# Kernel tuning notes

Hardware: AMD Instinct MI355X
Metric: run time of the kernel (lower is better)

Reference implementation:

```python
import jax, jax.numpy as jnp
import numpy as np

EMBED_DIM = 1024
NUM_MEMORY_SLOTS = 256
B, Q = 8, 4096


def setup_inputs() -> dict:
    key = jax.random.key(0)
    ks = jax.random.split(key, 6)
    s = 1.0 / np.sqrt(EMBED_DIM)
    return {
        "x": jax.random.normal(ks[0], (B, Q, EMBED_DIM), dtype=jnp.float32),
        "memory_bank": jax.random.normal(ks[1], (NUM_MEMORY_SLOTS, EMBED_DIM), dtype=jnp.float32),
        "Wq": jax.random.uniform(ks[2], (EMBED_DIM, EMBED_DIM), jnp.float32, -s, s),
        "bq": jax.random.uniform(ks[3], (EMBED_DIM,), jnp.float32, -s, s),
        "Wo": jax.random.uniform(ks[4], (EMBED_DIM, EMBED_DIM), jnp.float32, -s, s),
        "bo": jax.random.uniform(ks[5], (EMBED_DIM,), jnp.float32, -s, s),
    }


def reference(x, memory_bank, Wq, bq, Wo, bo):
    # query projection: [B,Q,E]
    queries = jnp.einsum('bqe,fe->bqf', x, Wq) + bq
    # attention over fixed memory bank: scores [B,Q,M]
    scores = jnp.einsum('bqe,me->bqm', queries, memory_bank)
    weights = jax.nn.softmax(scores, axis=-1)
    attended = jnp.einsum('bqm,me->bqe', weights, memory_bank)
    # output projection + residual
    return jnp.einsum('bqe,fe->bqf', attended, Wo) + bo + x
```

## Files before the change

### kernel.cpp

```cpp
#include <hip/hip_runtime.h>
#include <hip/hip_bf16.h>
#include <stdint.h>

#define TOK 32768
#define EMB 1024
#define MSL 256

typedef __attribute__((ext_vector_type(8))) short short8;
typedef __attribute__((ext_vector_type(4))) float f32x4;

__device__ __forceinline__ ushort f2bf(float f) {
    union { float f; uint32_t u; } c; c.f = f;
    uint32_t u = c.u;
    return (ushort)((u + 0x7fffu + ((u >> 16) & 1u)) >> 16);
}

__device__ __forceinline__ void split2(float f, ushort& h, ushort& l) {
    union { float f; uint32_t u; } c; c.f = f;
    h = (ushort)(c.u >> 16);
    union { uint32_t u; float f; } hv; hv.u = c.u & 0xffff0000u;
    union { float f; uint32_t u; } lc; lc.f = f - hv.f;
    l = (ushort)(lc.u >> 16);
}

__device__ __forceinline__ void async_copy16(const void* gsrc, void* ldst) {
    __builtin_amdgcn_global_load_lds(
        (const __attribute__((address_space(1))) uint32_t*)gsrc,
        (__attribute__((address_space(3))) uint32_t*)ldst,
        16, 0, 0);
}

__global__ __launch_bounds__(256) void zero_f32(float* __restrict__ p) {
    int i = blockIdx.x * 256 + threadIdx.x;
    ((float4*)p)[i] = float4{0.f, 0.f, 0.f, 0.f};
}

__global__ __launch_bounds__(256) void cast_f32_bf16(const float* __restrict__ in,
                                                     ushort* __restrict__ out) {
    int i = blockIdx.x * 256 + threadIdx.x;
    float4 v = ((const float4*)in)[i];
    ushort4 o;
    o.x = f2bf(v.x); o.y = f2bf(v.y); o.z = f2bf(v.z); o.w = f2bf(v.w);
    ((ushort4*)out)[i] = o;
}

__global__ __launch_bounds__(256) void split_f32(const float* __restrict__ in,
                                                 ushort* __restrict__ hi,
                                                 ushort* __restrict__ lo) {
    int i = blockIdx.x * 256 + threadIdx.x;
    float4 v = ((const float4*)in)[i];
    ushort4 h4, l4;
    split2(v.x, h4.x, l4.x); split2(v.y, h4.y, l4.y);
    split2(v.z, h4.z, l4.z); split2(v.w, h4.w, l4.w);
    ((ushort4*)hi)[i] = h4;
    ((ushort4*)lo)[i] = l4;
}

__global__ __launch_bounds__(256) void transpose_split(const float* __restrict__ in,
                                                       ushort* __restrict__ outh,
                                                       ushort* __restrict__ outl) {
    __shared__ float ld[64 * 65];
    const int t = threadIdx.x;
    const int eBase = blockIdx.x * 64;
    const int fBase = blockIdx.y * 64;
    #pragma unroll
    for (int r = 0; r < 16; ++r) {
        int row = r * 4 + (t >> 6);
        int col = t & 63;
        ld[row * 65 + col] = in[(size_t)(fBase + row) * EMB + eBase + col];
    }
    __syncthreads();
    #pragma unroll
    for (int r = 0; r < 16; ++r) {
        int row = r * 4 + (t >> 6);
        int col = t & 63;
        float v = ld[col * 65 + row];
        ushort h, l; split2(v, h, l);
        size_t o = (size_t)(eBase + row) * EMB + fBase + col;
        outh[o] = h; outl[o] = l;
    }
}

__global__ __launch_bounds__(256) void dot_c(const float* __restrict__ bq,
                                             const float* __restrict__ mb,
                                             float* __restrict__ c) {
    int m = blockIdx.x * 4 + (threadIdx.x >> 6);
    int lane = threadIdx.x & 63;
    const float4* mrow = (const float4*)(mb + (size_t)m * EMB);
    const float4* brow = (const float4*)bq;
    float s = 0.f;
    #pragma unroll
    for (int k = 0; k < 4; ++k) {
        float4 a = mrow[lane + k * 64];
        float4 b = brow[lane + k * 64];
        s += a.x * b.x + a.y * b.y + a.z * b.z + a.w * b.w;
    }
    #pragma unroll
    for (int off = 32; off; off >>= 1) s += __shfl_xor(s, off, 64);
    if (lane == 0) c[m] = s;
}


template<bool ADD_BIAS, bool OUT_BF16, bool ATOMIC>
__global__ __launch_bounds__(256) void gemm_s(
    const float* __restrict__ A, const ushort* __restrict__ Bh,
    const ushort* __restrict__ Bl, const float* __restrict__ bias,
    void* __restrict__ Cout, int K, int ldc)
{
    __shared__ ushort sAh[128 * 64];
    __shared__ ushort sAl[128 * 64];
    __shared__ ushort sBh[128 * 64];
    __shared__ ushort sBl[128 * 64];

    const int t = threadIdx.x;
    const int lane = t & 63;
    const int wave = t >> 6;
    const int wr = wave >> 1;
    const int wc = wave & 1;
    const int rowBase = blockIdx.y * 128;
    const int colBase = blockIdx.x * 128;

    const float*  Ab  = A  + (size_t)rowBase * K;
    const ushort* Bhb = Bh + (size_t)colBase * K;
    const ushort* Blb = Bl + (size_t)colBase * K;

    const int cg = ((t & 7) ^ ((t >> 3) & 7)) << 3;

    f32x4 acc[4][4] = {};

    const int kIters = (K >> 6) / (ATOMIC ? gridDim.z : 1);
    const int ktBase = ATOMIC ? blockIdx.z * kIters : 0;
    for (int kt = ktBase; kt < ktBase + kIters; ++kt) {
        const int k0 = kt << 6;
        __syncthreads();
        #pragma unroll
        for (int r = 0; r < 4; ++r) {
            int row = r * 32 + (t >> 3);
            async_copy16(Bhb + (size_t)row * K + k0 + cg, &sBh[(size_t)(r * 256 + wave * 64) * 8]);
            async_copy16(Blb + (size_t)row * K + k0 + cg, &sBl[(size_t)(r * 256 + wave * 64) * 8]);
        }
        #pragma unroll
        for (int r = 0; r < 4; ++r) {
            int i = r * 256 + t;
            int row = r * 32 + (t >> 3);
            const float* src = Ab + (size_t)row * K + k0 + cg;
            float4 f0 = *(const float4*)src;
            float4 f1 = *(const float4*)(src + 4);
            short8 hv, lv; ushort h, l;
            split2(f0.x, h, l); hv[0] = (short)h; lv[0] = (short)l;
            split2(f0.y, h, l); hv[1] = (short)h; lv[1] = (short)l;
            split2(f0.z, h, l); hv[2] = (short)h; lv[2] = (short)l;
            split2(f0.w, h, l); hv[3] = (short)h; lv[3] = (short)l;
            split2(f1.x, h, l); hv[4] = (short)h; lv[4] = (short)l;
            split2(f1.y, h, l); hv[5] = (short)h; lv[5] = (short)l;
            split2(f1.z, h, l); hv[6] = (short)h; lv[6] = (short)l;
            split2(f1.w, h, l); hv[7] = (short)h; lv[7] = (short)l;
            *(short8*)&sAh[(size_t)i * 8] = hv;
            *(short8*)&sAl[(size_t)i * 8] = lv;
        }
        __syncthreads();

        #pragma unroll
        for (int ks = 0; ks < 2; ++ks) {
            const int kc = ks * 4 + (lane >> 4);
            short8 ah[4], al[4], bh[4], bl[4];
            #pragma unroll
            for (int i2 = 0; i2 < 4; ++i2) {
                int row = wr * 64 + i2 * 16 + (lane & 15);
                int off = row * 64 + ((kc ^ (row & 7)) << 3);
                ah[i2] = *(const short8*)&sAh[off];
                al[i2] = *(const short8*)&sAl[off];
            }
            #pragma unroll
            for (int j = 0; j < 4; ++j) {
                int row = wc * 64 + j * 16 + (lane & 15);
                int off = row * 64 + ((kc ^ (row & 7)) << 3);
                bh[j] = *(const short8*)&sBh[off];
                bl[j] = *(const short8*)&sBl[off];
            }
            #pragma unroll
            for (int i2 = 0; i2 < 4; ++i2)
                #pragma unroll
                for (int j = 0; j < 4; ++j) {
                    acc[i2][j] = __builtin_amdgcn_mfma_f32_16x16x32_bf16(ah[i2], bh[j], acc[i2][j], 0, 0, 0);
                    acc[i2][j] = __builtin_amdgcn_mfma_f32_16x16x32_bf16(ah[i2], bl[j], acc[i2][j], 0, 0, 0);
                    acc[i2][j] = __builtin_amdgcn_mfma_f32_16x16x32_bf16(al[i2], bh[j], acc[i2][j], 0, 0, 0);
                }
        }
    }

    #pragma unroll
    for (int i2 = 0; i2 < 4; ++i2) {
        #pragma unroll
        for (int j = 0; j < 4; ++j) {
            const int col = colBase + wc * 64 + j * 16 + (lane & 15);
            float bcol = ADD_BIAS ? bias[col] : 0.0f;
            #pragma unroll
            for (int r = 0; r < 4; ++r) {
                const int row = rowBase + wr * 64 + i2 * 16 + ((lane >> 4) << 2) + r;
                float v = acc[i2][j][r] + bcol;
                if (ATOMIC)
                    atomicAdd(&((float*)Cout)[(size_t)row * ldc + col], v);
                else if (OUT_BF16)
                    ((ushort*)Cout)[(size_t)row * ldc + col] = f2bf(v);
                else
                    ((float*)Cout)[(size_t)row * ldc + col] = v;
            }
        }
    }
}

__global__ __launch_bounds__(512, 2) void fused_attn(
    const float* __restrict__ x, const ushort* __restrict__ Ph,
    const ushort* __restrict__ Pl, const float* __restrict__ cvec,
    const ushort* __restrict__ RTb, const float* __restrict__ bo,
    float* __restrict__ out)
{
    __shared__ ushort smem[65536];
    ushort* sAh = smem;
    ushort* sAl = smem + 8192;
    ushort* sBh = smem + 16384;
    ushort* sBl = smem + 32768;
    ushort* sW  = smem;
    float*  redM = (float*)&smem[49152];
    float*  redS = (float*)&smem[50176];

    const int t = threadIdx.x;
    const int lane = t & 63;
    const int wave = t >> 6;
    const int wr = wave >> 2;
    const int wc = wave & 3;
    const int rowBase = blockIdx.x * 128;

    const float* Ab = x + (size_t)rowBase * EMB;
    const int cg = ((t & 7) ^ ((t >> 3) & 7)) << 3;

    f32x4 acc[4][4] = {};

    for (int kt = 0; kt < 16; ++kt) {
        const int k0 = kt << 6;
        __syncthreads();
        #pragma unroll
        for (int r = 0; r < 4; ++r) {
            int row = r * 64 + (t >> 3);
            async_copy16(Ph + (size_t)row * EMB + k0 + cg, &sBh[(size_t)(r * 512 + wave * 64) * 8]);
            async_copy16(Pl + (size_t)row * EMB + k0 + cg, &sBl[(size_t)(r * 512 + wave * 64) * 8]);
        }
        #pragma unroll
        for (int r = 0; r < 2; ++r) {
            int i = r * 512 + t;
            int row = r * 64 + (t >> 3);
            const float* src = Ab + (size_t)row * EMB + k0 + cg;
            float4 f0 = *(const float4*)src;
            float4 f1 = *(const float4*)(src + 4);
            short8 hv, lv; ushort h, l;
            split2(f0.x, h, l); hv[0] = (short)h; lv[0] = (short)l;
            split2(f0.y, h, l); hv[1] = (short)h; lv[1] = (short)l;
            split2(f0.z, h, l); hv[2] = (short)h; lv[2] = (short)l;
            split2(f0.w, h, l); hv[3] = (short)h; lv[3] = (short)l;
            split2(f1.x, h, l); hv[4] = (short)h; lv[4] = (short)l;
            split2(f1.y, h, l); hv[5] = (short)h; lv[5] = (short)l;
            split2(f1.z, h, l); hv[6] = (short)h; lv[6] = (short)l;
            split2(f1.w, h, l); hv[7] = (short)h; lv[7] = (short)l;
            *(short8*)&sAh[(size_t)i * 8] = hv;
            *(short8*)&sAl[(size_t)i * 8] = lv;
        }
        __syncthreads();

        #pragma unroll
        for (int ks = 0; ks < 2; ++ks) {
            const int kc = ks * 4 + (lane >> 4);
            short8 ah[4], al[4], bh[4], bl[4];
            #pragma unroll
            for (int i2 = 0; i2 < 4; ++i2) {
                int row = wr * 64 + i2 * 16 + (lane & 15);
                int off = row * 64 + ((kc ^ (row & 7)) << 3);
                ah[i2] = *(const short8*)&sAh[off];
                al[i2] = *(const short8*)&sAl[off];
            }
            #pragma unroll
            for (int j = 0; j < 4; ++j) {
                int row = wc * 64 + j * 16 + (lane & 15);
                int off = row * 64 + ((kc ^ (row & 7)) << 3);
                bh[j] = *(const short8*)&sBh[off];
                bl[j] = *(const short8*)&sBl[off];
            }
            #pragma unroll
            for (int i2 = 0; i2 < 4; ++i2)
                #pragma unroll
                for (int j = 0; j < 4; ++j) {
                    acc[i2][j] = __builtin_amdgcn_mfma_f32_16x16x32_bf16(ah[i2], bh[j], acc[i2][j], 0, 0, 0);
                    acc[i2][j] = __builtin_amdgcn_mfma_f32_16x16x32_bf16(ah[i2], bl[j], acc[i2][j], 0, 0, 0);
                    acc[i2][j] = __builtin_amdgcn_mfma_f32_16x16x32_bf16(al[i2], bh[j], acc[i2][j], 0, 0, 0);
                }
        }
    }

    {
        float cj[4];
        #pragma unroll
        for (int j = 0; j < 4; ++j) cj[j] = cvec[wc * 64 + j * 16 + (lane & 15)];
        #pragma unroll
        for (int i2 = 0; i2 < 4; ++i2)
            #pragma unroll
            for (int j = 0; j < 4; ++j)
                #pragma unroll
                for (int r = 0; r < 4; ++r) acc[i2][j][r] += cj[j];
    }
    {
        float pmax[4][4];
        #pragma unroll
        for (int i2 = 0; i2 < 4; ++i2)
            #pragma unroll
            for (int r = 0; r < 4; ++r) {
                float m0 = fmaxf(fmaxf(acc[i2][0][r], acc[i2][1][r]),
                                 fmaxf(acc[i2][2][r], acc[i2][3][r]));
                #pragma unroll
                for (int off = 8; off; off >>= 1) m0 = fmaxf(m0, __shfl_xor(m0, off, 64));
                pmax[i2][r] = m0;
            }
        if ((lane & 15) == 0) {
            #pragma unroll
            for (int i2 = 0; i2 < 4; ++i2)
                #pragma unroll
                for (int r = 0; r < 4; ++r)
                    redM[wc * 128 + wr * 64 + i2 * 16 + ((lane >> 4) << 2) + r] = pmax[i2][r];
        }
    }
    __syncthreads();
    {
        float psum[4][4];
        #pragma unroll
        for (int i2 = 0; i2 < 4; ++i2)
            #pragma unroll
            for (int r = 0; r < 4; ++r) {
                int R = wr * 64 + i2 * 16 + ((lane >> 4) << 2) + r;
                float mx = fmaxf(fmaxf(redM[R], redM[128 + R]),
                                 fmaxf(redM[256 + R], redM[384 + R]));
                float s = 0.f;
                #pragma unroll
                for (int j = 0; j < 4; ++j) {
                    float e = __expf(acc[i2][j][r] - mx);
                    acc[i2][j][r] = e;
                    s += e;
                }
                #pragma unroll
                for (int off = 8; off; off >>= 1) s += __shfl_xor(s, off, 64);
                psum[i2][r] = s;
            }
        if ((lane & 15) == 0) {
            #pragma unroll
            for (int i2 = 0; i2 < 4; ++i2)
                #pragma unroll
                for (int r = 0; r < 4; ++r)
                    redS[wc * 128 + wr * 64 + i2 * 16 + ((lane >> 4) << 2) + r] = psum[i2][r];
        }
    }
    __syncthreads();
    #pragma unroll
    for (int i2 = 0; i2 < 4; ++i2)
        #pragma unroll
        for (int r = 0; r < 4; ++r) {
            int R = wr * 64 + i2 * 16 + ((lane >> 4) << 2) + r;
            float tot = redS[R] + redS[128 + R] + redS[256 + R] + redS[384 + R];
            float inv = 1.0f / tot;
            #pragma unroll
            for (int j = 0; j < 4; ++j) {
                int col = wc * 64 + j * 16 + (lane & 15);
                int cc = col >> 3;
                int slot = (cc & 24) | ((cc & 7) ^ (R & 7));
                sW[R * 256 + slot * 8 + (lane & 7)] = f2bf(acc[i2][j][r] * inv);
            }
        }

    auto stage_rt = [&](int fcn, int buf) {
        const ushort* src = RTb + (size_t)(fcn * 64) * MSL;
        ushort* dstb = smem + 32768 + buf * 16384;
        #pragma unroll
        for (int r = 0; r < 4; ++r) {
            int fr = r * 16 + (t >> 5);
            int c = t & 31;
            int gc = (c & 24) | ((c & 7) ^ (fr & 7));
            async_copy16(src + (size_t)fr * MSL + gc * 8,
                         &dstb[(size_t)(r * 512 + wave * 64) * 8]);
        }
    };
    stage_rt(0, 0);
    __syncthreads();

    const int wr2 = wave >> 1;
    const int wc2 = wave & 1;

    short8 af[2][8];
    #pragma unroll
    for (int i2 = 0; i2 < 2; ++i2) {
        int R = wr2 * 32 + i2 * 16 + (lane & 15);
        #pragma unroll
        for (int ks2 = 0; ks2 < 8; ++ks2) {
            int cc = ks2 * 4 + (lane >> 4);
            int slot = (cc & 24) | ((cc & 7) ^ (R & 7));
            af[i2][ks2] = *(const short8*)&sW[R * 256 + slot * 8];
        }
    }

    for (int fc = 0; fc < 16; ++fc) {
        if (fc < 15) stage_rt(fc + 1, (fc + 1) & 1);
        const ushort* bufp = smem + 32768 + (fc & 1) * 16384;
        f32x4 acc2[2][2] = {};
        #pragma unroll
        for (int ks2 = 0; ks2 < 8; ++ks2) {
            int cc = ks2 * 4 + (lane >> 4);
            short8 b[2];
            #pragma unroll
            for (int j = 0; j < 2; ++j) {
                int frow = wc2 * 32 + j * 16 + (lane & 15);
                int slot = (cc & 24) | ((cc & 7) ^ (frow & 7));
                b[j] = *(const short8*)&bufp[frow * 256 + slot * 8];
            }
            #pragma unroll
            for (int i2 = 0; i2 < 2; ++i2)
                #pragma unroll
                for (int j = 0; j < 2; ++j)
                    acc2[i2][j] = __builtin_amdgcn_mfma_f32_16x16x32_bf16(
                        af[i2][ks2], b[j], acc2[i2][j], 0, 0, 0);
        }
        #pragma unroll
        for (int i2 = 0; i2 < 2; ++i2)
            #pragma unroll
            for (int j = 0; j < 2; ++j) {
                int col = fc * 64 + wc2 * 32 + j * 16 + (lane & 15);
                float bcol = bo[col];
                #pragma unroll
                for (int r = 0; r < 4; ++r) {
                    int row = rowBase + wr2 * 32 + i2 * 16 + ((lane >> 4) << 2) + r;
                    out[(size_t)row * EMB + col] =
                        acc2[i2][j][r] + bcol + x[(size_t)row * EMB + col];
                }
            }
        __syncthreads();
    }
}

extern "C" void kernel_launch(void* const* d_in, const int* in_sizes, int n_in,
                              void* d_out, int out_size, void* d_ws, size_t ws_size,
                              hipStream_t stream) {
    const float* x  = (const float*)d_in[0];
    const float* mb = (const float*)d_in[1];
    const float* Wq = (const float*)d_in[2];
    const float* bq = (const float*)d_in[3];
    const float* Wo = (const float*)d_in[4];
    const float* bo = (const float*)d_in[5];
    float* out = (float*)d_out;

    char* ws = (char*)d_ws;
    size_t o = 0;
    float*  P    = (float*)(ws + o);  o += (size_t)MSL * EMB * 4;
    float*  RTf  = (float*)(ws + o);  o += (size_t)EMB * MSL * 4;
    ushort* mbh  = (ushort*)(ws + o); o += (size_t)MSL * EMB * 2;
    ushort* mbl  = (ushort*)(ws + o); o += (size_t)MSL * EMB * 2;
    ushort* wqth = (ushort*)(ws + o); o += (size_t)EMB * EMB * 2;
    ushort* wqtl = (ushort*)(ws + o); o += (size_t)EMB * EMB * 2;
    ushort* Ph   = (ushort*)(ws + o); o += (size_t)MSL * EMB * 2;
    ushort* Pl   = (ushort*)(ws + o); o += (size_t)MSL * EMB * 2;
    ushort* RTb  = (ushort*)(ws + o); o += (size_t)EMB * MSL * 2;
    float*  cvec = (float*)(ws + o);  o += (size_t)MSL * 4;

    zero_f32<<<(2 * MSL * EMB / 4) / 256, 256, 0, stream>>>(P);

    split_f32<<<(MSL * EMB / 4) / 256, 256, 0, stream>>>(mb, mbh, mbl);
    transpose_split<<<dim3(16, 16), 256, 0, stream>>>(Wq, wqth, wqtl);
    dot_c<<<MSL / 4, 256, 0, stream>>>(bq, mb, cvec);

    gemm_s<false, false, true><<<dim3(EMB / 128, MSL / 128, 16), 256, 0, stream>>>(
        mb, wqth, wqtl, nullptr, P, EMB, EMB);
    split_f32<<<(MSL * EMB / 4) / 256, 256, 0, stream>>>(P, Ph, Pl);

    gemm_s<false, false, true><<<dim3(MSL / 128, EMB / 128, 16), 256, 0, stream>>>(
        Wo, mbh, mbl, nullptr, RTf, EMB, MSL);
    cast_f32_bf16<<<(EMB * MSL / 4) / 256, 256, 0, stream>>>(RTf, RTb);

    fused_attn<<<TOK / 128, 512, 0, stream>>>(x, Ph, Pl, cvec, RTb, bo, out);
}
```

Before: 351.6 us.

## Merge preprocessing kernels, drop split-K atomics, shrink attention tile to 64 rows

Folds the transpose/split, mb split and bias-dot kernels into one launch. The two weight precompute GEMMs now run in a single 32-block launch with full K and no atomics, so the zeroing and post-cast kernels are no longer needed. The main fused attention kernel moves from 128-row, 512-thread blocks to 64-row, 256-thread blocks with less shared memory. Its output projection reads a fragment-ordered RT matrix straight from global memory instead of double-buffered LDS staging. Fewer launches and syncs are traded for a pre-GEMM stage that uses only 32 blocks, plus uncached global fragment loads repeated per block.

```diff
diff --git a/kernel.cpp b/kernel.cpp
--- a/kernel.cpp
+++ b/kernel.cpp
@@ -30,95 +30,79 @@
         16, 0, 0);
 }
 
-__global__ __launch_bounds__(256) void zero_f32(float* __restrict__ p) {
-    int i = blockIdx.x * 256 + threadIdx.x;
-    ((float4*)p)[i] = float4{0.f, 0.f, 0.f, 0.f};
-}
-
-__global__ __launch_bounds__(256) void cast_f32_bf16(const float* __restrict__ in,
-                                                     ushort* __restrict__ out) {
-    int i = blockIdx.x * 256 + threadIdx.x;
-    float4 v = ((const float4*)in)[i];
-    ushort4 o;
-    o.x = f2bf(v.x); o.y = f2bf(v.y); o.z = f2bf(v.z); o.w = f2bf(v.w);
-    ((ushort4*)out)[i] = o;
-}
-
-__global__ __launch_bounds__(256) void split_f32(const float* __restrict__ in,
-                                                 ushort* __restrict__ hi,
-                                                 ushort* __restrict__ lo) {
-    int i = blockIdx.x * 256 + threadIdx.x;
-    float4 v = ((const float4*)in)[i];
-    ushort4 h4, l4;
-    split2(v.x, h4.x, l4.x); split2(v.y, h4.y, l4.y);
-    split2(v.z, h4.z, l4.z); split2(v.w, h4.w, l4.w);
-    ((ushort4*)hi)[i] = h4;
-    ((ushort4*)lo)[i] = l4;
-}
-
-__global__ __launch_bounds__(256) void transpose_split(const float* __restrict__ in,
-                                                       ushort* __restrict__ outh,
-                                                       ushort* __restrict__ outl) {
+
+__global__ __launch_bounds__(256) void pre_small(
+    const float* __restrict__ Wq, ushort* __restrict__ wqth, ushort* __restrict__ wqtl,
+    const float* __restrict__ mb, ushort* __restrict__ mbh, ushort* __restrict__ mbl,
+    const float* __restrict__ bq, float* __restrict__ cvec)
+{
     __shared__ float ld[64 * 65];
+    const int b = blockIdx.x;
     const int t = threadIdx.x;
-    const int eBase = blockIdx.x * 64;
-    const int fBase = blockIdx.y * 64;
-    #pragma unroll
-    for (int r = 0; r < 16; ++r) {
-        int row = r * 4 + (t >> 6);
-        int col = t & 63;
-        ld[row * 65 + col] = in[(size_t)(fBase + row) * EMB + eBase + col];
-    }
-    __syncthreads();
-    #pragma unroll
-    for (int r = 0; r < 16; ++r) {
-        int row = r * 4 + (t >> 6);
-        int col = t & 63;
-        float v = ld[col * 65 + row];
-        ushort h, l; split2(v, h, l);
-        size_t o = (size_t)(eBase + row) * EMB + fBase + col;
-        outh[o] = h; outl[o] = l;
-    }
-}
-
-__global__ __launch_bounds__(256) void dot_c(const float* __restrict__ bq,
-                                             const float* __restrict__ mb,
-                                             float* __restrict__ c) {
-    int m = blockIdx.x * 4 + (threadIdx.x >> 6);
-    int lane = threadIdx.x & 63;
-    const float4* mrow = (const float4*)(mb + (size_t)m * EMB);
-    const float4* brow = (const float4*)bq;
-    float s = 0.f;
-    #pragma unroll
-    for (int k = 0; k < 4; ++k) {
-        float4 a = mrow[lane + k * 64];
-        float4 b = brow[lane + k * 64];
-        s += a.x * b.x + a.y * b.y + a.z * b.z + a.w * b.w;
-    }
-    #pragma unroll
-    for (int off = 32; off; off >>= 1) s += __shfl_xor(s, off, 64);
-    if (lane == 0) c[m] = s;
-}
-
-
-template<bool ADD_BIAS, bool OUT_BF16, bool ATOMIC>
-__global__ __launch_bounds__(256) void gemm_s(
-    const float* __restrict__ A, const ushort* __restrict__ Bh,
-    const ushort* __restrict__ Bl, const float* __restrict__ bias,
-    void* __restrict__ Cout, int K, int ldc)
+    if (b < 256) {
+        const int eBase = (b & 15) * 64;
+        const int fBase = (b >> 4) * 64;
+        #pragma unroll
+        for (int r = 0; r < 16; ++r) {
+            int row = r * 4 + (t >> 6);
+            int col = t & 63;
+            ld[row * 65 + col] = Wq[(size_t)(fBase + row) * EMB + eBase + col];
+        }
+        __syncthreads();
+        #pragma unroll
+        for (int r = 0; r < 16; ++r) {
+            int row = r * 4 + (t >> 6);
+            int col = t & 63;
+            float v = ld[col * 65 + row];
+            ushort h, l; split2(v, h, l);
+            size_t o = (size_t)(eBase + row) * EMB + fBase + col;
+            wqth[o] = h; wqtl[o] = l;
+        }
+    } else if (b < 512) {
+        int i = (b - 256) * 256 + t;
+        float4 v = ((const float4*)mb)[i];
+        ushort4 h4, l4;
+        split2(v.x, h4.x, l4.x); split2(v.y, h4.y, l4.y);
+        split2(v.z, h4.z, l4.z); split2(v.w, h4.w, l4.w);
+        ((ushort4*)mbh)[i] = h4;
+        ((ushort4*)mbl)[i] = l4;
+    } else {
+        int m = (b - 512) * 4 + (t >> 6);
+        int lane = t & 63;
+        const float4* mrow = (const float4*)(mb + (size_t)m * EMB);
+        const float4* brow = (const float4*)bq;
+        float s = 0.f;
+        #pragma unroll
+        for (int k = 0; k < 4; ++k) {
+            float4 a = mrow[lane + k * 64];
+            float4 bb = brow[lane + k * 64];
+            s += a.x * bb.x + a.y * bb.y + a.z * bb.z + a.w * bb.w;
+        }
+        #pragma unroll
+        for (int off = 32; off; off >>= 1) s += __shfl_xor(s, off, 64);
+        if (lane == 0) cvec[m] = s;
+    }
+}
+
+template<int MODE>
+__device__ __forceinline__ void gemm_body(
+    ushort* smem, const float* __restrict__ A,
+    const ushort* __restrict__ Bh, const ushort* __restrict__ Bl,
+    ushort* __restrict__ O1, ushort* __restrict__ O2,
+    int K, int ldc, int bx, int by)
 {
-    __shared__ ushort sAh[128 * 64];
-    __shared__ ushort sAl[128 * 64];
-    __shared__ ushort sBh[128 * 64];
-    __shared__ ushort sBl[128 * 64];
+    ushort* sAh = smem;
+    ushort* sAl = smem + 8192;
+    ushort* sBh = smem + 16384;
+    ushort* sBl = smem + 24576;
 
     const int t = threadIdx.x;
     const int lane = t & 63;
     const int wave = t >> 6;
     const int wr = wave >> 1;
     const int wc = wave & 1;
-    const int rowBase = blockIdx.y * 128;
-    const int colBase = blockIdx.x * 128;
+    const int rowBase = by * 128;
+    const int colBase = bx * 128;
 
     const float*  Ab  = A  + (size_t)rowBase * K;
     const ushort* Bhb = Bh + (size_t)colBase * K;
@@ -128,9 +112,8 @@
 
     f32x4 acc[4][4] = {};
 
-    const int kIters = (K >> 6) / (ATOMIC ? gridDim.z : 1);
-    const int ktBase = ATOMIC ? blockIdx.z * kIters : 0;
-    for (int kt = ktBase; kt < ktBase + kIters; ++kt) {
+    const int kIters = K >> 6;
+    for (int kt = 0; kt < kIters; ++kt) {
         const int k0 = kt << 6;
         __syncthreads();
         #pragma unroll
@@ -194,43 +177,60 @@
         #pragma unroll
         for (int j = 0; j < 4; ++j) {
             const int col = colBase + wc * 64 + j * 16 + (lane & 15);
-            float bcol = ADD_BIAS ? bias[col] : 0.0f;
             #pragma unroll
             for (int r = 0; r < 4; ++r) {
                 const int row = rowBase + wr * 64 + i2 * 16 + ((lane >> 4) << 2) + r;
-                float v = acc[i2][j][r] + bcol;
-                if (ATOMIC)
-                    atomicAdd(&((float*)Cout)[(size_t)row * ldc + col], v);
-                else if (OUT_BF16)
-                    ((ushort*)Cout)[(size_t)row * ldc + col] = f2bf(v);
-                else
-                    ((float*)Cout)[(size_t)row * ldc + col] = v;
-            }
-        }
-    }
-}
-
-__global__ __launch_bounds__(512, 2) void fused_attn(
+                float v = acc[i2][j][r];
+                if (MODE == 0) {
+                    ushort h, l; split2(v, h, l);
+                    O1[(size_t)row * ldc + col] = h;
+                    O2[(size_t)row * ldc + col] = l;
+                } else {
+                    int fc = row >> 6, jj = (row & 63) >> 4, lanelo = row & 15;
+                    int cc = col >> 3, ksx = cc >> 2, lanehi = cc & 3, e = col & 7;
+                    size_t idx = ((((size_t)fc * 8 + ksx) * 4 + jj) * 64 + lanehi * 16 + lanelo) * 8 + e;
+                    O1[idx] = f2bf(v);
+                }
+            }
+        }
+    }
+}
+
+__global__ __launch_bounds__(256) void pre_gemms(
+    const float* __restrict__ mb, const ushort* __restrict__ wqth, const ushort* __restrict__ wqtl,
+    const float* __restrict__ Wo, const ushort* __restrict__ mbh, const ushort* __restrict__ mbl,
+    ushort* __restrict__ Ph, ushort* __restrict__ Pl, ushort* __restrict__ RTfrag)
+{
+    __shared__ ushort smem[32768];
+    const int b = blockIdx.x;
+    if (b < 16) {
+        gemm_body<0>(smem, mb, wqth, wqtl, Ph, Pl, EMB, EMB, b & 7, b >> 3);
+    } else {
+        const int id = b - 16;
+        gemm_body<1>(smem, Wo, mbh, mbl, RTfrag, nullptr, EMB, 0, id & 1, id >> 1);
+    }
+}
+
+__global__ __launch_bounds__(256, 2) void fused_attn(
     const float* __restrict__ x, const ushort* __restrict__ Ph,
     const ushort* __restrict__ Pl, const float* __restrict__ cvec,
-    const ushort* __restrict__ RTb, const float* __restrict__ bo,
+    const ushort* __restrict__ RTfrag, const float* __restrict__ bo,
     float* __restrict__ out)
 {
-    __shared__ ushort smem[65536];
+    __shared__ ushort smem[40960];
     ushort* sAh = smem;
-    ushort* sAl = smem + 8192;
-    ushort* sBh = smem + 16384;
-    ushort* sBl = smem + 32768;
+    ushort* sAl = smem + 4096;
+    ushort* sBh = smem + 8192;
+    ushort* sBl = smem + 24576;
     ushort* sW  = smem;
-    float*  redM = (float*)&smem[49152];
-    float*  redS = (float*)&smem[50176];
+    float*  redM = (float*)&smem[39936];
+    float*  redS = (float*)&smem[40448];
 
     const int t = threadIdx.x;
     const int lane = t & 63;
     const int wave = t >> 6;
-    const int wr = wave >> 2;
-    const int wc = wave & 3;
-    const int rowBase = blockIdx.x * 128;
+    const int wc = wave;
+    const int rowBase = blockIdx.x * 64;
 
     const float* Ab = x + (size_t)rowBase * EMB;
     const int cg = ((t & 7) ^ ((t >> 3) & 7)) << 3;
@@ -241,15 +241,15 @@
         const int k0 = kt << 6;
         __syncthreads();
         #pragma unroll
-        for (int r = 0; r < 4; ++r) {
-            int row = r * 64 + (t >> 3);
-            async_copy16(Ph + (size_t)row * EMB + k0 + cg, &sBh[(size_t)(r * 512 + wave * 64) * 8]);
-            async_copy16(Pl + (size_t)row * EMB + k0 + cg, &sBl[(size_t)(r * 512 + wave * 64) * 8]);
+        for (int r = 0; r < 8; ++r) {
+            int row = r * 32 + (t >> 3);
+            async_copy16(Ph + (size_t)row * EMB + k0 + cg, &sBh[(size_t)(r * 256 + wave * 64) * 8]);
+            async_copy16(Pl + (size_t)row * EMB + k0 + cg, &sBl[(size_t)(r * 256 + wave * 64) * 8]);
         }
         #pragma unroll
         for (int r = 0; r < 2; ++r) {
-            int i = r * 512 + t;
-            int row = r * 64 + (t >> 3);
+            int i = r * 256 + t;
+            int row = r * 32 + (t >> 3);
             const float* src = Ab + (size_t)row * EMB + k0 + cg;
             float4 f0 = *(const float4*)src;
             float4 f1 = *(const float4*)(src + 4);
@@ -273,7 +273,7 @@
             short8 ah[4], al[4], bh[4], bl[4];
             #pragma unroll
             for (int i2 = 0; i2 < 4; ++i2) {
-                int row = wr * 64 + i2 * 16 + (lane & 15);
+                int row = i2 * 16 + (lane & 15);
                 int off = row * 64 + ((kc ^ (row & 7)) << 3);
                 ah[i2] = *(const short8*)&sAh[off];
                 al[i2] = *(const short8*)&sAl[off];
@@ -307,25 +307,24 @@
                 #pragma unroll
                 for (int r = 0; r < 4; ++r) acc[i2][j][r] += cj[j];
     }
-    {
-        float pmax[4][4];
+    float pmax[4][4];
+    #pragma unroll
+    for (int i2 = 0; i2 < 4; ++i2)
+        #pragma unroll
+        for (int r = 0; r < 4; ++r) {
+            float m0 = fmaxf(fmaxf(acc[i2][0][r], acc[i2][1][r]),
+                             fmaxf(acc[i2][2][r], acc[i2][3][r]));
+            #pragma unroll
+            for (int off = 8; off; off >>= 1) m0 = fmaxf(m0, __shfl_xor(m0, off, 64));
+            pmax[i2][r] = m0;
+        }
+    __syncthreads();
+    if ((lane & 15) == 0) {
         #pragma unroll
         for (int i2 = 0; i2 < 4; ++i2)
             #pragma unroll
-            for (int r = 0; r < 4; ++r) {
-                float m0 = fmaxf(fmaxf(acc[i2][0][r], acc[i2][1][r]),
-                                 fmaxf(acc[i2][2][r], acc[i2][3][r]));
-                #pragma unroll
-                for (int off = 8; off; off >>= 1) m0 = fmaxf(m0, __shfl_xor(m0, off, 64));
-                pmax[i2][r] = m0;
-            }
-        if ((lane & 15) == 0) {
-            #pragma unroll
-            for (int i2 = 0; i2 < 4; ++i2)
-                #pragma unroll
-                for (int r = 0; r < 4; ++r)
-                    redM[wc * 128 + wr * 64 + i2 * 16 + ((lane >> 4) << 2) + r] = pmax[i2][r];
-        }
+            for (int r = 0; r < 4; ++r)
+                redM[wc * 64 + i2 * 16 + ((lane >> 4) << 2) + r] = pmax[i2][r];
     }
     __syncthreads();
     {
@@ -334,9 +333,9 @@
         for (int i2 = 0; i2 < 4; ++i2)
             #pragma unroll
             for (int r = 0; r < 4; ++r) {
-                int R = wr * 64 + i2 * 16 + ((lane >> 4) << 2) + r;
-                float mx = fmaxf(fmaxf(redM[R], redM[128 + R]),
-                                 fmaxf(redM[256 + R], redM[384 + R]));
+                int R = i2 * 16 + ((lane >> 4) << 2) + r;
+                float mx = fmaxf(fmaxf(redM[R], redM[64 + R]),
+                                 fmaxf(redM[128 + R], redM[192 + R]));
                 float s = 0.f;
                 #pragma unroll
                 for (int j = 0; j < 4; ++j) {
@@ -353,7 +352,7 @@
             for (int i2 = 0; i2 < 4; ++i2)
                 #pragma unroll
                 for (int r = 0; r < 4; ++r)
-                    redS[wc * 128 + wr * 64 + i2 * 16 + ((lane >> 4) << 2) + r] = psum[i2][r];
+                    redS[wc * 64 + i2 * 16 + ((lane >> 4) << 2) + r] = psum[i2][r];
         }
     }
     __syncthreads();
@@ -361,8 +360,8 @@
     for (int i2 = 0; i2 < 4; ++i2)
         #pragma unroll
         for (int r = 0; r < 4; ++r) {
-            int R = wr * 64 + i2 * 16 + ((lane >> 4) << 2) + r;
-            float tot = redS[R] + redS[128 + R] + redS[256 + R] + redS[384 + R];
+            int R = i2 * 16 + ((lane >> 4) << 2) + r;
+            float tot = redS[R] + redS[64 + R] + redS[128 + R] + redS[192 + R];
             float inv = 1.0f / tot;
             #pragma unroll
             for (int j = 0; j < 4; ++j) {
@@ -372,20 +371,6 @@
                 sW[R * 256 + slot * 8 + (lane & 7)] = f2bf(acc[i2][j][r] * inv);
             }
         }
-
-    auto stage_rt = [&](int fcn, int buf) {
-        const ushort* src = RTb + (size_t)(fcn * 64) * MSL;
-        ushort* dstb = smem + 32768 + buf * 16384;
-        #pragma unroll
-        for (int r = 0; r < 4; ++r) {
-            int fr = r * 16 + (t >> 5);
-            int c = t & 31;
-            int gc = (c & 24) | ((c & 7) ^ (fr & 7));
-            async_copy16(src + (size_t)fr * MSL + gc * 8,
-                         &dstb[(size_t)(r * 512 + wave * 64) * 8]);
-        }
-    };
-    stage_rt(0, 0);
     __syncthreads();
 
     const int wr2 = wave >> 1;
@@ -396,33 +381,29 @@
     for (int i2 = 0; i2 < 2; ++i2) {
         int R = wr2 * 32 + i2 * 16 + (lane & 15);
         #pragma unroll
-        for (int ks2 = 0; ks2 < 8; ++ks2) {
-            int cc = ks2 * 4 + (lane >> 4);
+        for (int ks = 0; ks < 8; ++ks) {
+            int cc = ks * 4 + (lane >> 4);
             int slot = (cc & 24) | ((cc & 7) ^ (R & 7));
-            af[i2][ks2] = *(const short8*)&sW[R * 256 + slot * 8];
+            af[i2][ks] = *(const short8*)&sW[R * 256 + slot * 8];
         }
     }
 
     for (int fc = 0; fc < 16; ++fc) {
-        if (fc < 15) stage_rt(fc + 1, (fc + 1) & 1);
-        const ushort* bufp = smem + 32768 + (fc & 1) * 16384;
         f32x4 acc2[2][2] = {};
         #pragma unroll
-        for (int ks2 = 0; ks2 < 8; ++ks2) {
-            int cc = ks2 * 4 + (lane >> 4);
+        for (int ks = 0; ks < 8; ++ks) {
             short8 b[2];
             #pragma unroll
             for (int j = 0; j < 2; ++j) {
-                int frow = wc2 * 32 + j * 16 + (lane & 15);
-                int slot = (cc & 24) | ((cc & 7) ^ (frow & 7));
-                b[j] = *(const short8*)&bufp[frow * 256 + slot * 8];
+                int jj = wc2 * 2 + j;
+                b[j] = *(const short8*)&RTfrag[((((size_t)fc * 8 + ks) * 4 + jj) * 64 + lane) * 8];
             }
             #pragma unroll
             for (int i2 = 0; i2 < 2; ++i2)
                 #pragma unroll
                 for (int j = 0; j < 2; ++j)
                     acc2[i2][j] = __builtin_amdgcn_mfma_f32_16x16x32_bf16(
-                        af[i2][ks2], b[j], acc2[i2][j], 0, 0, 0);
+                        af[i2][ks], b[j], acc2[i2][j], 0, 0, 0);
         }
         #pragma unroll
         for (int i2 = 0; i2 < 2; ++i2)
@@ -437,7 +418,6 @@
                         acc2[i2][j][r] + bcol + x[(size_t)row * EMB + col];
                 }
             }
-        __syncthreads();
     }
 }
 
@@ -454,30 +434,18 @@
 
     char* ws = (char*)d_ws;
     size_t o = 0;
-    float*  P    = (float*)(ws + o);  o += (size_t)MSL * EMB * 4;
-    float*  RTf  = (float*)(ws + o);  o += (size_t)EMB * MSL * 4;
-    ushort* mbh  = (ushort*)(ws + o); o += (size_t)MSL * EMB * 2;
-    ushort* mbl  = (ushort*)(ws + o); o += (size_t)MSL * EMB * 2;
-    ushort* wqth = (ushort*)(ws + o); o += (size_t)EMB * EMB * 2;
-    ushort* wqtl = (ushort*)(ws + o); o += (size_t)EMB * EMB * 2;
-    ushort* Ph   = (ushort*)(ws + o); o += (size_t)MSL * EMB * 2;
-    ushort* Pl   = (ushort*)(ws + o); o += (size_t)MSL * EMB * 2;
-    ushort* RTb  = (ushort*)(ws + o); o += (size_t)EMB * MSL * 2;
-    float*  cvec = (float*)(ws + o);  o += (size_t)MSL * 4;
-
-    zero_f32<<<(2 * MSL * EMB / 4) / 256, 256, 0, stream>>>(P);
-
-    split_f32<<<(MSL * EMB / 4) / 256, 256, 0, stream>>>(mb, mbh, mbl);
-    transpose_split<<<dim3(16, 16), 256, 0, stream>>>(Wq, wqth, wqtl);
-    dot_c<<<MSL / 4, 256, 0, stream>>>(bq, mb, cvec);
-
-    gemm_s<false, false, true><<<dim3(EMB / 128, MSL / 128, 16), 256, 0, stream>>>(
-        mb, wqth, wqtl, nullptr, P, EMB, EMB);
-    split_f32<<<(MSL * EMB / 4) / 256, 256, 0, stream>>>(P, Ph, Pl);
-
-    gemm_s<false, false, true><<<dim3(MSL / 128, EMB / 128, 16), 256, 0, stream>>>(
-        Wo, mbh, mbl, nullptr, RTf, EMB, MSL);
-    cast_f32_bf16<<<(EMB * MSL / 4) / 256, 256, 0, stream>>>(RTf, RTb);
-
-    fused_attn<<<TOK / 128, 512, 0, stream>>>(x, Ph, Pl, cvec, RTb, bo, out);
-}
+    ushort* mbh    = (ushort*)(ws + o); o += (size_t)MSL * EMB * 2;
+    ushort* mbl    = (ushort*)(ws + o); o += (size_t)MSL * EMB * 2;
+    ushort* wqth   = (ushort*)(ws + o); o += (size_t)EMB * EMB * 2;
+    ushort* wqtl   = (ushort*)(ws + o); o += (size_t)EMB * EMB * 2;
+    ushort* Ph     = (ushort*)(ws + o); o += (size_t)MSL * EMB * 2;
+    ushort* Pl     = (ushort*)(ws + o); o += (size_t)MSL * EMB * 2;
+    ushort* RTfrag = (ushort*)(ws + o); o += (size_t)EMB * MSL * 2;
+    float*  cvec   = (float*)(ws + o);  o += (size_t)MSL * 4;
+
+    pre_small<<<576, 256, 0, stream>>>(Wq, wqth, wqtl, mb, mbh, mbl, bq, cvec);
+
+    pre_gemms<<<32, 256, 0, stream>>>(mb, wqth, wqtl, Wo, mbh, mbl, Ph, Pl, RTfrag);
+
+    fused_attn<<<TOK / 64, 256, 0, stream>>>(x, Ph, Pl, cvec, RTfrag, bo, out);
+}
```

After: 350.7 us. No clear change (-0.3%).
